# Performance work log

Hardware: AMD Instinct MI355X
Metric: run time of the kernel (lower is better)

Reference implementation:

```python
import jax, jax.numpy as jnp
import numpy as np

N_USERS = 100000
N_ENTITIES = 50000
D = 64
NNZ = 2000000


def setup_inputs() -> dict:
    key = jax.random.key(0)
    k1, k2, k3, k4, k5 = jax.random.split(key, 5)
    return {
        "user_emb": jax.random.normal(k1, (N_USERS, D), dtype=jnp.float32),
        "entity_emb": jax.random.normal(k2, (N_ENTITIES, D), dtype=jnp.float32),
        "rows": jax.random.randint(k3, (NNZ,), 0, N_USERS, dtype=jnp.int32),
        "cols": jax.random.randint(k4, (NNZ,), 0, N_ENTITIES, dtype=jnp.int32),
        "vals": jax.random.uniform(k5, (NNZ,), dtype=jnp.float32),
    }


def reference(user_emb, entity_emb, rows, cols, vals):
    # interact_mat is COO sparse [n_users, n_entities] with (rows, cols, vals).
    # entity_agg = interact_mat.T @ user_emb : scatter-add user rows into entity bins
    entity_agg = jax.ops.segment_sum(
        vals[:, None] * user_emb[rows], cols, num_segments=entity_emb.shape[0]
    )
    # user_agg = interact_mat @ entity_emb : scatter-add entity rows into user bins
    user_agg = jax.ops.segment_sum(
        vals[:, None] * entity_emb[cols], rows, num_segments=user_emb.shape[0]
    )
    return entity_agg, user_agg
```

## Files before the change

kernel.cpp:

```cpp
#include <hip/hip_runtime.h>

#define DIM 64
#define PBITS 7
#define PART_BUCKETS 128
#define NPART_MAX 1184
#define EPT 32
#define EPB (EPT * 256)
#define CAP2 8192

__global__ void coo_scatter_kernel(const float* __restrict__ user_emb,
                                   const float* __restrict__ entity_emb,
                                   const int* __restrict__ rows,
                                   const int* __restrict__ cols,
                                   const float* __restrict__ vals,
                                   float* __restrict__ entity_agg,
                                   float* __restrict__ user_agg,
                                   int nnz) {
    long long tid = (long long)blockIdx.x * blockDim.x + threadIdx.x;
    long long total = (long long)nnz * DIM;
    if (tid >= total) return;
    int edge = (int)(tid >> 6);
    int d = (int)(tid & 63);
    int r = rows[edge];
    int c = cols[edge];
    float v = vals[edge];
    atomicAdd(&entity_agg[c * DIM + d], v * user_emb[r * DIM + d]);
    atomicAdd(&user_agg[r * DIM + d], v * entity_emb[c * DIM + d]);
}


__global__ __launch_bounds__(256) void pass0_hist(const int* __restrict__ rows,
                                                  const int* __restrict__ cols,
                                                  int* __restrict__ pcnt,
                                                  int ne, int nnz, int npart) {
    __shared__ int h[NPART_MAX];
    for (int t = threadIdx.x; t < npart; t += 256) h[t] = 0;
    __syncthreads();
    for (int i = blockIdx.x * blockDim.x + threadIdx.x; i < nnz;
         i += gridDim.x * blockDim.x) {
        int c = cols[i];
        int r = rows[i];
        atomicAdd(&h[c >> PBITS], 1);
        atomicAdd(&h[(ne + r) >> PBITS], 1);
    }
    __syncthreads();
    for (int t = threadIdx.x; t < npart; t += 256)
        if (h[t]) atomicAdd(&pcnt[t], h[t]);
}

__global__ __launch_bounds__(256) void scan_parts(const int* __restrict__ pcnt,
                                                  int* __restrict__ poffs,
                                                  int* __restrict__ pcursor,
                                                  int* __restrict__ ovfcnt,
                                                  int npart) {
    __shared__ int sh[256];
    int t = threadIdx.x;
    int local[8];
    int s = 0;
#pragma unroll
    for (int j = 0; j < 8; ++j) {
        int idx = t * 8 + j;
        local[j] = (idx < npart) ? pcnt[idx] : 0;
        s += local[j];
    }
    sh[t] = s;
    for (int off = 1; off < 256; off <<= 1) {
        __syncthreads();
        int tmp = (t >= off) ? sh[t - off] : 0;
        __syncthreads();
        sh[t] += tmp;
    }
    __syncthreads();
    int run = sh[t] - s;
#pragma unroll
    for (int j = 0; j < 8; ++j) {
        int idx = t * 8 + j;
        if (idx < npart) {
            poffs[idx] = run;
            pcursor[idx] = run;
            run += local[j];
        }
    }
    if (t == 255) poffs[npart] = sh[255];
    if (t == 0) *ovfcnt = 0;
}

__global__ __launch_bounds__(256) void pass1_part(const int* __restrict__ rows,
                                                  const int* __restrict__ cols,
                                                  const float* __restrict__ vals,
                                                  int* __restrict__ pcursor,
                                                  uint2* __restrict__ payload,
                                                  int ne, int nnz, int npart) {
    __shared__ int hist[NPART_MAX];
    __shared__ int cur[NPART_MAX];
    __shared__ int gbase[NPART_MAX];
    for (int t = threadIdx.x; t < npart; t += 256) { hist[t] = 0; cur[t] = 0; }
    __syncthreads();

    int base = blockIdx.x * EPB;
#pragma unroll 4
    for (int k = 0; k < EPT; ++k) {
        int i = base + threadIdx.x + k * 256;
        if (i < nnz) {
            atomicAdd(&hist[cols[i] >> PBITS], 1);
            atomicAdd(&hist[(ne + rows[i]) >> PBITS], 1);
        }
    }
    __syncthreads();
    for (int p = threadIdx.x; p < npart; p += 256) {
        int c_ = hist[p];
        if (c_) gbase[p] = atomicAdd(&pcursor[p], c_);
    }
    __syncthreads();
#pragma unroll 4
    for (int k = 0; k < EPT; ++k) {
        int i = base + threadIdx.x + k * 256;
        if (i < nnz) {
            int r = rows[i];
            int c = cols[i];
            unsigned vb = __float_as_uint(vals[i]);
            int b2 = ne + r;
            int p1 = c >> PBITS;
            int p2 = b2 >> PBITS;
            int rank1 = atomicAdd(&cur[p1], 1);
            payload[(size_t)gbase[p1] + rank1] =
                make_uint2(((unsigned)(c & (PART_BUCKETS - 1)) << 18) | (unsigned)r, vb);
            int rank2 = atomicAdd(&cur[p2], 1);
            payload[(size_t)gbase[p2] + rank2] =
                make_uint2(((unsigned)(b2 & (PART_BUCKETS - 1)) << 18) | (1u << 17) | (unsigned)c, vb);
        }
    }
}

__global__ __launch_bounds__(256) void pass2_sort(uint2* __restrict__ payload,
                                                  const int* __restrict__ poffs,
                                                  int* __restrict__ offs,
                                                  int* __restrict__ ends,
                                                  int* __restrict__ ovfcnt,
                                                  int* __restrict__ ovflist) {
    __shared__ int h[PART_BUCKETS], sc[PART_BUCKETS], cu[PART_BUCKETS];
    int p = blockIdx.x;
    int beg = poffs[p];
    int n = poffs[p + 1] - beg;
    int t = threadIdx.x;
    if (t < PART_BUCKETS) h[t] = 0;
    __syncthreads();

    if (n > CAP2) {
        if (t == 0) {
            int o = atomicAdd(ovfcnt, 1);
            ovflist[o] = p;
        }
        if (t < PART_BUCKETS) {
            offs[p * PART_BUCKETS + t] = beg;
            ends[p * PART_BUCKETS + t] = beg;
        }
        return;
    }

    uint2 rec[32];
#pragma unroll
    for (int k = 0; k < 32; ++k) {
        int idx = t + k * 256;
        if (idx < n) {
            rec[k] = payload[(size_t)beg + idx];
            atomicAdd(&h[(rec[k].x >> 18) & (PART_BUCKETS - 1)], 1);
        }
    }
    __syncthreads();
    if (t == 0) {
        int run = 0;
#pragma unroll
        for (int j = 0; j < PART_BUCKETS; ++j) { sc[j] = run; run += h[j]; }
    }
    __syncthreads();
    if (t < PART_BUCKETS) {
        offs[p * PART_BUCKETS + t] = beg + sc[t];
        ends[p * PART_BUCKETS + t] = beg + sc[t] + h[t];
        cu[t] = sc[t];
    }
    __syncthreads();
#pragma unroll
    for (int k = 0; k < 32; ++k) {
        int idx = t + k * 256;
        if (idx < n) {
            int bucket = (rec[k].x >> 18) & (PART_BUCKETS - 1);
            int rank = atomicAdd(&cu[bucket], 1);
            payload[(size_t)beg + rank] = rec[k];
        }
    }
}

__global__ __launch_bounds__(256) void agg_buckets(const float* __restrict__ user_emb,
                                                   const float* __restrict__ entity_emb,
                                                   const int* __restrict__ offs,
                                                   const int* __restrict__ ends,
                                                   const uint2* __restrict__ payload,
                                                   float* __restrict__ out,
                                                   int nbuckets) {
    int bucket = blockIdx.x * 4 + (threadIdx.x >> 6);
    int lane = threadIdx.x & 63;
    if (bucket >= nbuckets) return;
    int beg = offs[bucket];
    int end = ends[bucket];

    int grp = lane >> 4;
    int sub = lane & 15;

    float ax0 = 0.f, ay0 = 0.f, az0 = 0.f, aw0 = 0.f;
    float ax1 = 0.f, ay1 = 0.f, az1 = 0.f, aw1 = 0.f;
    float ax2 = 0.f, ay2 = 0.f, az2 = 0.f, aw2 = 0.f;
    float ax3 = 0.f, ay3 = 0.f, az3 = 0.f, aw3 = 0.f;

    int i = beg;
    for (; i + 16 <= end; i += 16) {
        uint2 r0 = payload[i + grp];
        uint2 r1 = payload[i + 4 + grp];
        uint2 r2 = payload[i + 8 + grp];
        uint2 r3 = payload[i + 12 + grp];
        const float* __restrict__ t0 = (r0.x & (1u << 17)) ? entity_emb : user_emb;
        const float* __restrict__ t1 = (r1.x & (1u << 17)) ? entity_emb : user_emb;
        const float* __restrict__ t2 = (r2.x & (1u << 17)) ? entity_emb : user_emb;
        const float* __restrict__ t3 = (r3.x & (1u << 17)) ? entity_emb : user_emb;
        const float4 e0 = *(const float4*)(t0 + (size_t)(r0.x & 0x1FFFFu) * DIM + sub * 4);
        const float4 e1 = *(const float4*)(t1 + (size_t)(r1.x & 0x1FFFFu) * DIM + sub * 4);
        const float4 e2 = *(const float4*)(t2 + (size_t)(r2.x & 0x1FFFFu) * DIM + sub * 4);
        const float4 e3 = *(const float4*)(t3 + (size_t)(r3.x & 0x1FFFFu) * DIM + sub * 4);
        float v0 = __uint_as_float(r0.y);
        float v1 = __uint_as_float(r1.y);
        float v2 = __uint_as_float(r2.y);
        float v3 = __uint_as_float(r3.y);
        ax0 += v0 * e0.x; ay0 += v0 * e0.y; az0 += v0 * e0.z; aw0 += v0 * e0.w;
        ax1 += v1 * e1.x; ay1 += v1 * e1.y; az1 += v1 * e1.z; aw1 += v1 * e1.w;
        ax2 += v2 * e2.x; ay2 += v2 * e2.y; az2 += v2 * e2.z; aw2 += v2 * e2.w;
        ax3 += v3 * e3.x; ay3 += v3 * e3.y; az3 += v3 * e3.z; aw3 += v3 * e3.w;
    }
    for (; i + 8 <= end; i += 8) {
        uint2 rA = payload[i + grp];
        uint2 rB = payload[i + 4 + grp];
        const float* __restrict__ tA = (rA.x & (1u << 17)) ? entity_emb : user_emb;
        const float* __restrict__ tB = (rB.x & (1u << 17)) ? entity_emb : user_emb;
        const float4 eA = *(const float4*)(tA + (size_t)(rA.x & 0x1FFFFu) * DIM + sub * 4);
        const float4 eB = *(const float4*)(tB + (size_t)(rB.x & 0x1FFFFu) * DIM + sub * 4);
        float vA = __uint_as_float(rA.y);
        float vB = __uint_as_float(rB.y);
        ax0 += vA * eA.x; ay0 += vA * eA.y; az0 += vA * eA.z; aw0 += vA * eA.w;
        ax1 += vB * eB.x; ay1 += vB * eB.y; az1 += vB * eB.z; aw1 += vB * eB.w;
    }
    for (; i < end; i += 4) {
        int j = i + grp;
        bool valid = j < end;
        uint2 r = payload[valid ? j : end - 1];
        const float* __restrict__ t = (r.x & (1u << 17)) ? entity_emb : user_emb;
        const float4 e = *(const float4*)(t + (size_t)(r.x & 0x1FFFFu) * DIM + sub * 4);
        float v = valid ? __uint_as_float(r.y) : 0.f;
        ax0 += v * e.x; ay0 += v * e.y; az0 += v * e.z; aw0 += v * e.w;
    }

    ax0 += ax1 + ax2 + ax3; ay0 += ay1 + ay2 + ay3;
    az0 += az1 + az2 + az3; aw0 += aw1 + aw2 + aw3;
    ax0 += __shfl_xor(ax0, 16, 64); ay0 += __shfl_xor(ay0, 16, 64);
    az0 += __shfl_xor(az0, 16, 64); aw0 += __shfl_xor(aw0, 16, 64);
    ax0 += __shfl_xor(ax0, 32, 64); ay0 += __shfl_xor(ay0, 32, 64);
    az0 += __shfl_xor(az0, 32, 64); aw0 += __shfl_xor(aw0, 32, 64);

    if (grp == 0) {
        float4 res = make_float4(ax0, ay0, az0, aw0);
        *(float4*)(out + (size_t)bucket * DIM + sub * 4) = res;
    }
}

__global__ void pass3_ovf(const uint2* __restrict__ payload,
                          const int* __restrict__ poffs,
                          const int* __restrict__ ovfcnt,
                          const int* __restrict__ ovflist,
                          const float* __restrict__ user_emb,
                          const float* __restrict__ entity_emb,
                          float* __restrict__ out) {
    int no = *ovfcnt;
    for (int o = 0; o < no; ++o) {
        int p = ovflist[o];
        int beg = poffs[p];
        int n = poffs[p + 1] - beg;
        for (int j = blockIdx.x * blockDim.x + threadIdx.x; j < n * 16;
             j += gridDim.x * blockDim.x) {
            uint2 rec = payload[(size_t)beg + (j >> 4)];
            int d4 = (j & 15) * 4;
            const float* tab = (rec.x & (1u << 17)) ? entity_emb : user_emb;
            float v = __uint_as_float(rec.y);
            int bucket = (p << PBITS) | (int)((rec.x >> 18) & (PART_BUCKETS - 1));
            const float* src = tab + (size_t)(rec.x & 0x1FFFFu) * DIM + d4;
            float* dst = out + (size_t)bucket * DIM + d4;
            for (int d = 0; d < 4; ++d) atomicAdd(&dst[d], v * src[d]);
        }
    }
}

extern "C" void kernel_launch(void* const* d_in, const int* in_sizes, int n_in,
                              void* d_out, int out_size, void* d_ws, size_t ws_size,
                              hipStream_t stream) {
    const float* user_emb   = (const float*)d_in[0];
    const float* entity_emb = (const float*)d_in[1];
    const int*   rows       = (const int*)d_in[2];
    const int*   cols       = (const int*)d_in[3];
    const float* vals       = (const float*)d_in[4];
    int nnz = in_sizes[2];
    int nu  = in_sizes[0] / DIM;
    int ne  = in_sizes[1] / DIM;
    int nb  = ne + nu;
    int npart = (nb + PART_BUCKETS - 1) / PART_BUCKETS;
    int nbk_pad = npart * PART_BUCKETS;

    float* out = (float*)d_out;

    size_t n_ints = (size_t)npart * 3 + 1 + (size_t)nbk_pad * 2 + 1 + npart;
    size_t pay_off_ints = (n_ints + 1) & ~(size_t)1;
    size_t need = pay_off_ints * 4 + (size_t)2 * nnz * 8;

    if (ws_size < need || npart > NPART_MAX || nu > 131072 || ne > 131072) {
        float* entity_agg = out;
        float* user_agg   = out + (size_t)ne * DIM;
        hipMemsetAsync(d_out, 0, (size_t)out_size * sizeof(float), stream);
        long long total = (long long)nnz * DIM;
        int block = 256;
        long long grid = (total + block - 1) / block;
        coo_scatter_kernel<<<(int)grid, block, 0, stream>>>(
            user_emb, entity_emb, rows, cols, vals, entity_agg, user_agg, nnz);
        return;
    }

    int*   pcnt    = (int*)d_ws;
    int*   poffs   = pcnt + npart;
    int*   pcursor = poffs + npart + 1;
    int*   offs    = pcursor + npart;
    int*   ends    = offs + nbk_pad;
    int*   ovfcnt  = ends + nbk_pad;
    int*   ovflist = ovfcnt + 1;
    uint2* payload = (uint2*)((int*)d_ws + pay_off_ints);

    hipMemsetAsync(pcnt, 0, (size_t)npart * sizeof(int), stream);

    pass0_hist<<<512, 256, 0, stream>>>(rows, cols, pcnt, ne, nnz, npart);
    scan_parts<<<1, 256, 0, stream>>>(pcnt, poffs, pcursor, ovfcnt, npart);
    int g1 = (nnz + EPB - 1) / EPB;
    pass1_part<<<g1, 256, 0, stream>>>(rows, cols, vals, pcursor, payload, ne, nnz, npart);
    pass2_sort<<<npart, 256, 0, stream>>>(payload, poffs, offs, ends, ovfcnt, ovflist);
    int gAgg = (nb + 3) / 4;
    agg_buckets<<<gAgg, 256, 0, stream>>>(user_emb, entity_emb, offs, ends, payload, out, nb);
    pass3_ovf<<<64, 256, 0, stream>>>(payload, poffs, ovfcnt, ovflist, user_emb, entity_emb, out);
}
```

Before: 235.7 us.

## Fuse per-partition bucket sort with aggregation using shared-memory records

Merges the partition sort pass and the bucket aggregation kernel into one kernel. Each block sorts its partition's records in LDS and then aggregates its 64 buckets directly. Partitions shrink from 128 to 64 buckets so the records fit in shared memory. This drops the global write-back of sorted payload, the offs/ends arrays and one launch. In exchange each block needs 32KB of LDS, which can limit occupancy, and each wave works through 16 buckets one after another, which may reduce memory-level parallelism on the embedding gathers.

```diff
diff --git a/kernel.cpp b/kernel.cpp
--- a/kernel.cpp
+++ b/kernel.cpp
@@ -1,12 +1,12 @@
 #include <hip/hip_runtime.h>
 
 #define DIM 64
-#define PBITS 7
-#define PART_BUCKETS 128
-#define NPART_MAX 1184
+#define PBITS 6
+#define PART_BUCKETS 64
+#define NPART_MAX 2368
 #define EPT 32
 #define EPB (EPT * 256)
-#define CAP2 8192
+#define CAP 4096
 
 __global__ void coo_scatter_kernel(const float* __restrict__ user_emb,
                                    const float* __restrict__ entity_emb,
@@ -55,11 +55,11 @@
                                                   int npart) {
     __shared__ int sh[256];
     int t = threadIdx.x;
-    int local[8];
+    int local[10];
     int s = 0;
 #pragma unroll
-    for (int j = 0; j < 8; ++j) {
-        int idx = t * 8 + j;
+    for (int j = 0; j < 10; ++j) {
+        int idx = t * 10 + j;
         local[j] = (idx < npart) ? pcnt[idx] : 0;
         s += local[j];
     }
@@ -73,8 +73,8 @@
     __syncthreads();
     int run = sh[t] - s;
 #pragma unroll
-    for (int j = 0; j < 8; ++j) {
-        int idx = t * 8 + j;
+    for (int j = 0; j < 10; ++j) {
+        int idx = t * 10 + j;
         if (idx < npart) {
             poffs[idx] = run;
             pcursor[idx] = run;
@@ -132,12 +132,15 @@
     }
 }
 
-__global__ __launch_bounds__(256) void pass2_sort(uint2* __restrict__ payload,
-                                                  const int* __restrict__ poffs,
-                                                  int* __restrict__ offs,
-                                                  int* __restrict__ ends,
-                                                  int* __restrict__ ovfcnt,
-                                                  int* __restrict__ ovflist) {
+__global__ __launch_bounds__(256) void sort_agg(const float* __restrict__ user_emb,
+                                                const float* __restrict__ entity_emb,
+                                                const uint2* __restrict__ payload,
+                                                const int* __restrict__ poffs,
+                                                int* __restrict__ ovfcnt,
+                                                int* __restrict__ ovflist,
+                                                float* __restrict__ out,
+                                                int nb) {
+    __shared__ uint2 srec[CAP];
     __shared__ int h[PART_BUCKETS], sc[PART_BUCKETS], cu[PART_BUCKETS];
     int p = blockIdx.x;
     int beg = poffs[p];
@@ -146,21 +149,22 @@
     if (t < PART_BUCKETS) h[t] = 0;
     __syncthreads();
 
-    if (n > CAP2) {
+    if (n > CAP) {
         if (t == 0) {
             int o = atomicAdd(ovfcnt, 1);
             ovflist[o] = p;
         }
-        if (t < PART_BUCKETS) {
-            offs[p * PART_BUCKETS + t] = beg;
-            ends[p * PART_BUCKETS + t] = beg;
+        int b0 = p << PBITS;
+        for (int e = t; e < PART_BUCKETS * DIM; e += 256) {
+            int b = b0 + (e >> 6);
+            if (b < nb) out[(size_t)b * DIM + (e & 63)] = 0.f;
         }
         return;
     }
 
-    uint2 rec[32];
-#pragma unroll
-    for (int k = 0; k < 32; ++k) {
+    uint2 rec[CAP / 256];
+#pragma unroll
+    for (int k = 0; k < CAP / 256; ++k) {
         int idx = t + k * 256;
         if (idx < n) {
             rec[k] = payload[(size_t)beg + idx];
@@ -171,102 +175,67 @@
     if (t == 0) {
         int run = 0;
 #pragma unroll
-        for (int j = 0; j < PART_BUCKETS; ++j) { sc[j] = run; run += h[j]; }
-    }
-    __syncthreads();
-    if (t < PART_BUCKETS) {
-        offs[p * PART_BUCKETS + t] = beg + sc[t];
-        ends[p * PART_BUCKETS + t] = beg + sc[t] + h[t];
-        cu[t] = sc[t];
-    }
-    __syncthreads();
-#pragma unroll
-    for (int k = 0; k < 32; ++k) {
+        for (int j = 0; j < PART_BUCKETS; ++j) { sc[j] = run; cu[j] = run; run += h[j]; }
+    }
+    __syncthreads();
+#pragma unroll
+    for (int k = 0; k < CAP / 256; ++k) {
         int idx = t + k * 256;
         if (idx < n) {
-            int bucket = (rec[k].x >> 18) & (PART_BUCKETS - 1);
-            int rank = atomicAdd(&cu[bucket], 1);
-            payload[(size_t)beg + rank] = rec[k];
-        }
-    }
-}
-
-__global__ __launch_bounds__(256) void agg_buckets(const float* __restrict__ user_emb,
-                                                   const float* __restrict__ entity_emb,
-                                                   const int* __restrict__ offs,
-                                                   const int* __restrict__ ends,
-                                                   const uint2* __restrict__ payload,
-                                                   float* __restrict__ out,
-                                                   int nbuckets) {
-    int bucket = blockIdx.x * 4 + (threadIdx.x >> 6);
-    int lane = threadIdx.x & 63;
-    if (bucket >= nbuckets) return;
-    int beg = offs[bucket];
-    int end = ends[bucket];
-
+            int b = (rec[k].x >> 18) & (PART_BUCKETS - 1);
+            int rank = atomicAdd(&cu[b], 1);
+            srec[rank] = rec[k];
+        }
+    }
+    __syncthreads();
+
+    int wid = t >> 6;
+    int lane = t & 63;
     int grp = lane >> 4;
     int sub = lane & 15;
 
-    float ax0 = 0.f, ay0 = 0.f, az0 = 0.f, aw0 = 0.f;
-    float ax1 = 0.f, ay1 = 0.f, az1 = 0.f, aw1 = 0.f;
-    float ax2 = 0.f, ay2 = 0.f, az2 = 0.f, aw2 = 0.f;
-    float ax3 = 0.f, ay3 = 0.f, az3 = 0.f, aw3 = 0.f;
-
-    int i = beg;
-    for (; i + 16 <= end; i += 16) {
-        uint2 r0 = payload[i + grp];
-        uint2 r1 = payload[i + 4 + grp];
-        uint2 r2 = payload[i + 8 + grp];
-        uint2 r3 = payload[i + 12 + grp];
-        const float* __restrict__ t0 = (r0.x & (1u << 17)) ? entity_emb : user_emb;
-        const float* __restrict__ t1 = (r1.x & (1u << 17)) ? entity_emb : user_emb;
-        const float* __restrict__ t2 = (r2.x & (1u << 17)) ? entity_emb : user_emb;
-        const float* __restrict__ t3 = (r3.x & (1u << 17)) ? entity_emb : user_emb;
-        const float4 e0 = *(const float4*)(t0 + (size_t)(r0.x & 0x1FFFFu) * DIM + sub * 4);
-        const float4 e1 = *(const float4*)(t1 + (size_t)(r1.x & 0x1FFFFu) * DIM + sub * 4);
-        const float4 e2 = *(const float4*)(t2 + (size_t)(r2.x & 0x1FFFFu) * DIM + sub * 4);
-        const float4 e3 = *(const float4*)(t3 + (size_t)(r3.x & 0x1FFFFu) * DIM + sub * 4);
-        float v0 = __uint_as_float(r0.y);
-        float v1 = __uint_as_float(r1.y);
-        float v2 = __uint_as_float(r2.y);
-        float v3 = __uint_as_float(r3.y);
-        ax0 += v0 * e0.x; ay0 += v0 * e0.y; az0 += v0 * e0.z; aw0 += v0 * e0.w;
-        ax1 += v1 * e1.x; ay1 += v1 * e1.y; az1 += v1 * e1.z; aw1 += v1 * e1.w;
-        ax2 += v2 * e2.x; ay2 += v2 * e2.y; az2 += v2 * e2.z; aw2 += v2 * e2.w;
-        ax3 += v3 * e3.x; ay3 += v3 * e3.y; az3 += v3 * e3.z; aw3 += v3 * e3.w;
-    }
-    for (; i + 8 <= end; i += 8) {
-        uint2 rA = payload[i + grp];
-        uint2 rB = payload[i + 4 + grp];
-        const float* __restrict__ tA = (rA.x & (1u << 17)) ? entity_emb : user_emb;
-        const float* __restrict__ tB = (rB.x & (1u << 17)) ? entity_emb : user_emb;
-        const float4 eA = *(const float4*)(tA + (size_t)(rA.x & 0x1FFFFu) * DIM + sub * 4);
-        const float4 eB = *(const float4*)(tB + (size_t)(rB.x & 0x1FFFFu) * DIM + sub * 4);
-        float vA = __uint_as_float(rA.y);
-        float vB = __uint_as_float(rB.y);
-        ax0 += vA * eA.x; ay0 += vA * eA.y; az0 += vA * eA.z; aw0 += vA * eA.w;
-        ax1 += vB * eB.x; ay1 += vB * eB.y; az1 += vB * eB.z; aw1 += vB * eB.w;
-    }
-    for (; i < end; i += 4) {
-        int j = i + grp;
-        bool valid = j < end;
-        uint2 r = payload[valid ? j : end - 1];
-        const float* __restrict__ t = (r.x & (1u << 17)) ? entity_emb : user_emb;
-        const float4 e = *(const float4*)(t + (size_t)(r.x & 0x1FFFFu) * DIM + sub * 4);
-        float v = valid ? __uint_as_float(r.y) : 0.f;
-        ax0 += v * e.x; ay0 += v * e.y; az0 += v * e.z; aw0 += v * e.w;
-    }
-
-    ax0 += ax1 + ax2 + ax3; ay0 += ay1 + ay2 + ay3;
-    az0 += az1 + az2 + az3; aw0 += aw1 + aw2 + aw3;
-    ax0 += __shfl_xor(ax0, 16, 64); ay0 += __shfl_xor(ay0, 16, 64);
-    az0 += __shfl_xor(az0, 16, 64); aw0 += __shfl_xor(aw0, 16, 64);
-    ax0 += __shfl_xor(ax0, 32, 64); ay0 += __shfl_xor(ay0, 32, 64);
-    az0 += __shfl_xor(az0, 32, 64); aw0 += __shfl_xor(aw0, 32, 64);
-
-    if (grp == 0) {
-        float4 res = make_float4(ax0, ay0, az0, aw0);
-        *(float4*)(out + (size_t)bucket * DIM + sub * 4) = res;
+    for (int bi = 0; bi < 16; ++bi) {
+        int lb = wid * 16 + bi;
+        int bucket = (p << PBITS) + lb;
+        int rb = sc[lb];
+        int cnt = h[lb];
+
+        float ax0 = 0.f, ay0 = 0.f, az0 = 0.f, aw0 = 0.f;
+        float ax1 = 0.f, ay1 = 0.f, az1 = 0.f, aw1 = 0.f;
+
+        int i = 0;
+        for (; i + 8 <= cnt; i += 8) {
+            uint2 rA = srec[rb + i + grp];
+            uint2 rB = srec[rb + i + 4 + grp];
+            const float* __restrict__ tA = (rA.x & (1u << 17)) ? entity_emb : user_emb;
+            const float* __restrict__ tB = (rB.x & (1u << 17)) ? entity_emb : user_emb;
+            const float4 eA = *(const float4*)(tA + (size_t)(rA.x & 0x1FFFFu) * DIM + sub * 4);
+            const float4 eB = *(const float4*)(tB + (size_t)(rB.x & 0x1FFFFu) * DIM + sub * 4);
+            float vA = __uint_as_float(rA.y);
+            float vB = __uint_as_float(rB.y);
+            ax0 += vA * eA.x; ay0 += vA * eA.y; az0 += vA * eA.z; aw0 += vA * eA.w;
+            ax1 += vB * eB.x; ay1 += vB * eB.y; az1 += vB * eB.z; aw1 += vB * eB.w;
+        }
+        for (; i < cnt; i += 4) {
+            int j = i + grp;
+            bool valid = j < cnt;
+            uint2 r = srec[rb + (valid ? j : cnt - 1)];
+            const float* __restrict__ tb = (r.x & (1u << 17)) ? entity_emb : user_emb;
+            const float4 e = *(const float4*)(tb + (size_t)(r.x & 0x1FFFFu) * DIM + sub * 4);
+            float v = valid ? __uint_as_float(r.y) : 0.f;
+            ax0 += v * e.x; ay0 += v * e.y; az0 += v * e.z; aw0 += v * e.w;
+        }
+
+        ax0 += ax1; ay0 += ay1; az0 += az1; aw0 += aw1;
+        ax0 += __shfl_xor(ax0, 16, 64); ay0 += __shfl_xor(ay0, 16, 64);
+        az0 += __shfl_xor(az0, 16, 64); aw0 += __shfl_xor(aw0, 16, 64);
+        ax0 += __shfl_xor(ax0, 32, 64); ay0 += __shfl_xor(ay0, 32, 64);
+        az0 += __shfl_xor(az0, 32, 64); aw0 += __shfl_xor(aw0, 32, 64);
+
+        if (grp == 0 && bucket < nb) {
+            float4 res = make_float4(ax0, ay0, az0, aw0);
+            *(float4*)(out + (size_t)bucket * DIM + sub * 4) = res;
+        }
     }
 }
 
@@ -309,11 +278,10 @@
     int ne  = in_sizes[1] / DIM;
     int nb  = ne + nu;
     int npart = (nb + PART_BUCKETS - 1) / PART_BUCKETS;
-    int nbk_pad = npart * PART_BUCKETS;
 
     float* out = (float*)d_out;
 
-    size_t n_ints = (size_t)npart * 3 + 1 + (size_t)nbk_pad * 2 + 1 + npart;
+    size_t n_ints = (size_t)npart * 4 + 2;
     size_t pay_off_ints = (n_ints + 1) & ~(size_t)1;
     size_t need = pay_off_ints * 4 + (size_t)2 * nnz * 8;
 
@@ -332,9 +300,7 @@
     int*   pcnt    = (int*)d_ws;
     int*   poffs   = pcnt + npart;
     int*   pcursor = poffs + npart + 1;
-    int*   offs    = pcursor + npart;
-    int*   ends    = offs + nbk_pad;
-    int*   ovfcnt  = ends + nbk_pad;
+    int*   ovfcnt  = pcursor + npart;
     int*   ovflist = ovfcnt + 1;
     uint2* payload = (uint2*)((int*)d_ws + pay_off_ints);
 
@@ -344,8 +310,8 @@
     scan_parts<<<1, 256, 0, stream>>>(pcnt, poffs, pcursor, ovfcnt, npart);
     int g1 = (nnz + EPB - 1) / EPB;
     pass1_part<<<g1, 256, 0, stream>>>(rows, cols, vals, pcursor, payload, ne, nnz, npart);
-    pass2_sort<<<npart, 256, 0, stream>>>(payload, poffs, offs, ends, ovfcnt, ovflist);
-    int gAgg = (nb + 3) / 4;
-    agg_buckets<<<gAgg, 256, 0, stream>>>(user_emb, entity_emb, offs, ends, payload, out, nb);
-    pass3_ovf<<<64, 256, 0, stream>>>(payload, poffs, ovfcnt, ovflist, user_emb, entity_emb, out);
-}
+    sort_agg<<<npart, 256, 0, stream>>>(user_emb, entity_emb, payload, poffs,
+                                        ovfcnt, ovflist, out, nb);
+    pass3_ovf<<<64, 256, 0, stream>>>(payload, poffs, ovfcnt, ovflist,
+                                      user_emb, entity_emb, out);
+}
```

Result: slower. 241.2 us (+2.4%).
